# Performance work log

Hardware: AMD Instinct MI355X
Metric: run time of the kernel (lower is better)

## Reference

```python
import jax, jax.numpy as jnp
import numpy as np

B, S, D, H, FF, R, NB = 8, 1024, 768, 12, 3072, 16, 768


def _ln(x, g, b, eps=1e-6):
    m = x.mean(-1, keepdims=True)
    v = jnp.mean((x - m) ** 2, axis=-1, keepdims=True)
    return (x - m) * jax.lax.rsqrt(v + eps) * g + b


def setup_inputs() -> dict:
    key = jax.random.key(0)

    def rn(i, shape, s=0.02):
        return jax.random.normal(jax.random.fold_in(key, i), shape, jnp.float32) * s

    inp = {
        "x": jax.random.normal(jax.random.fold_in(key, 0), (B, S, D), jnp.float32),
        "attn_mask": jnp.zeros((S, S), jnp.float32),
        "norm1_g": jnp.ones((D,), jnp.float32),
        "norm1_b": jnp.zeros((D,), jnp.float32),
        "q_w": rn(1, (D, D)), "q_b": jnp.zeros((D,), jnp.float32),
        "k_w": rn(2, (D, D)), "k_b": jnp.zeros((D,), jnp.float32),
        "v_w": rn(3, (D, D)), "v_b": jnp.zeros((D,), jnp.float32),
        "o_w": rn(4, (D, D)), "o_b": jnp.zeros((D,), jnp.float32),
        "norm2_g": jnp.ones((D,), jnp.float32),
        "norm2_b": jnp.zeros((D,), jnp.float32),
        "fc1_w": rn(5, (FF, D)), "fc1_b": jnp.zeros((FF,), jnp.float32),
        "fc2_w": rn(6, (D, FF)), "fc2_b": jnp.zeros((D,), jnp.float32),
        # shared LoRA (backbone tokens)
        "lora1_A": rn(7, (D, R)), "lora1_B": rn(8, (R, FF)),
        "lora2_A": rn(9, (FF, R)), "lora2_B": rn(10, (R, D)),
        # expert VeRA: frozen shared A/B, per-expert diagonal scaling vectors
        "vera1_A": rn(11, (D, R)), "vera1_B": rn(12, (R, FF)),
        "vera2_A": rn(13, (FF, R)), "vera2_B": rn(14, (R, D)),
        "expert_fc1_d": rn(15, (R,), 1.0), "expert_fc1_b": rn(16, (FF,), 1.0),
        "expert_fc2_d": rn(17, (R,), 1.0), "expert_fc2_b": rn(18, (D,), 1.0),
        "num_backbone_tokens": NB,
    }
    return inp


def reference(x, attn_mask, norm1_g, norm1_b, q_w, q_b, k_w, k_b, v_w, v_b,
              o_w, o_b, norm2_g, norm2_b, fc1_w, fc1_b, fc2_w, fc2_b,
              lora1_A, lora1_B, lora2_A, lora2_B,
              vera1_A, vera1_B, vera2_A, vera2_B,
              expert_fc1_d, expert_fc1_b, expert_fc2_d, expert_fc2_b,
              num_backbone_tokens):
    bsz, seq, dim = x.shape
    hd = dim // H                      # head_dim = 64
    scale = hd ** -0.5
    nb = num_backbone_tokens

    # ---- attention (manual bmm + mask + softmax, eval-mode dropout = identity) ----
    h = _ln(x, norm1_g, norm1_b)
    q = (h @ q_w.T + q_b).reshape(bsz, seq, H, hd)
    k = (h @ k_w.T + k_b).reshape(bsz, seq, H, hd)
    v = (h @ v_w.T + v_b).reshape(bsz, seq, H, hd)
    scores = jnp.einsum('bqhd,bkhd->bhqk', q * scale, k) + attn_mask  # [B,H,S,S]
    probs = jax.nn.softmax(scores, axis=-1)
    ao = jnp.einsum('bhqk,bkhd->bqhd', probs, v).reshape(bsz, seq, dim)
    x = x + (ao @ o_w.T + o_b)

    # ---- MLP with split backbone (shared LoRA) / expert (VeRA) adapters ----
    residual = x
    n2 = _ln(x, norm2_g, norm2_b)
    hid = n2 @ fc1_w.T + fc1_b                                   # [B,S,FF]
    hid_b = hid[:, :nb] + (n2[:, :nb] @ lora1_A) @ lora1_B
    hid_e = hid[:, nb:] + (((n2[:, nb:] @ vera1_A) * expert_fc1_d) @ vera1_B) * expert_fc1_b
    hid = jnp.concatenate([hid_b, hid_e], axis=1)
    hid = jax.nn.gelu(hid)
    out = hid @ fc2_w.T + fc2_b                                  # [B,S,D]
    out_b = out[:, :nb] + (hid[:, :nb] @ lora2_A) @ lora2_B
    out_e = out[:, nb:] + (((hid[:, nb:] @ vera2_A) * expert_fc2_d) @ vera2_B) * expert_fc2_b
    out = jnp.concatenate([out_b, out_e], axis=1)
    return residual + out
```

## Files before the change

kernel.cpp:

```cpp
#include <hip/hip_runtime.h>
#include <stdint.h>

#define B_  8
#define S_  1024
#define D_  768
#define H_  12
#define HD_ 64
#define FF_ 3072
#define M_  (B_*S_)
#define R_  16
#define QLD 2304
#define KBLK 128

typedef unsigned short u16;
typedef short s16x8 __attribute__((ext_vector_type(8)));
typedef float fx4  __attribute__((ext_vector_type(4)));

__device__ __forceinline__ float b2f(u16 u) {
  union { unsigned int i; float f; } c; c.i = ((unsigned int)u) << 16; return c.f;
}
__device__ __forceinline__ u16 f2b(float f) {
  union { float f; unsigned int i; } c; c.f = f;
  unsigned int x = c.i;
  x += 0x7FFFu + ((x >> 16) & 1u);
  return (u16)(x >> 16);
}
__device__ __forceinline__ float gelu_f(float x) {
  float u = 0.7978845608028654f * (x + 0.044715f * x * x * x);
  float e = __expf(2.f * u);
  float t = 1.f - 2.f / (e + 1.f);
  return 0.5f * x * (1.f + t);
}
__device__ __forceinline__ void gload16(const u16* gsrc, u16* ldst) {
  __builtin_amdgcn_global_load_lds(
      (__attribute__((address_space(1))) void*)(gsrc),
      (__attribute__((address_space(3))) void*)(ldst), 16, 0, 0);
}

__global__ __launch_bounds__(256)
void cvt_all(const float* __restrict__ q_w, const float* __restrict__ k_w,
             const float* __restrict__ v_w, const float* __restrict__ o_w,
             const float* __restrict__ fc1_w, const float* __restrict__ fc2_w,
             u16* __restrict__ wqkv, u16* __restrict__ wo,
             u16* __restrict__ wfc1, u16* __restrict__ wfc2)
{
  const int i = blockIdx.x * 256 + threadIdx.x;
  const int q1  = D_ * D_ / 4;
  const int fd4 = FF_ * D_ / 4;
  const float* s; u16* d; int j;
  if      (i <     q1)       { s = q_w;   d = wqkv;            j = i; }
  else if (i < 2 * q1)       { s = k_w;   d = wqkv + D_*D_;    j = i - q1; }
  else if (i < 3 * q1)       { s = v_w;   d = wqkv + 2*D_*D_;  j = i - 2*q1; }
  else if (i < 4 * q1)       { s = o_w;   d = wo;              j = i - 3*q1; }
  else if (i < 4 * q1 + fd4) { s = fc1_w; d = wfc1;            j = i - 4*q1; }
  else                       { s = fc2_w; d = wfc2;            j = i - 4*q1 - fd4; }
  const float4 f = ((const float4*)s)[j];
  ushort4 o4; o4.x = f2b(f.x); o4.y = f2b(f.y); o4.z = f2b(f.z); o4.w = f2b(f.w);
  ((ushort4*)d)[j] = o4;
}

__global__ __launch_bounds__(256)
void prep_all(const float* __restrict__ q_bv, const float* __restrict__ k_bv,
              const float* __restrict__ v_bv, float* __restrict__ qkvb,
              const float* __restrict__ lora1B, const float* __restrict__ vera1B,
              const float* __restrict__ e1b, u16* __restrict__ up1L, u16* __restrict__ up1V,
              const float* __restrict__ lora2B, const float* __restrict__ vera2B,
              const float* __restrict__ e2b, u16* __restrict__ up2L, u16* __restrict__ up2V,
              const float* __restrict__ lora2A, const float* __restrict__ vera2A,
              u16* __restrict__ a2tL, u16* __restrict__ a2tV)
{
  const int f = blockIdx.x * 256 + threadIdx.x;
  if (f < QLD)
    qkvb[f] = (f < D_) ? q_bv[f] : (f < 2 * D_) ? k_bv[f - D_] : v_bv[f - 2 * D_];
  {
    const float ev = e1b[f];
    #pragma unroll
    for (int r = 0; r < 16; ++r) {
      up1L[(size_t)f * 32 + r] = f2b(lora1B[(size_t)r * FF_ + f]);
      up1V[(size_t)f * 32 + r] = f2b(vera1B[(size_t)r * FF_ + f] * ev);
      up1L[(size_t)f * 32 + 16 + r] = 0;
      up1V[(size_t)f * 32 + 16 + r] = 0;
    }
  }
  {
    const float4* apl = (const float4*)(lora2A + (size_t)f * 16);
    const float4* apv = (const float4*)(vera2A + (size_t)f * 16);
    #pragma unroll
    for (int q4 = 0; q4 < 4; ++q4) {
      const float4 l4 = apl[q4], v4 = apv[q4];
      a2tL[(size_t)(q4*4+0) * FF_ + f] = f2b(l4.x);
      a2tL[(size_t)(q4*4+1) * FF_ + f] = f2b(l4.y);
      a2tL[(size_t)(q4*4+2) * FF_ + f] = f2b(l4.z);
      a2tL[(size_t)(q4*4+3) * FF_ + f] = f2b(l4.w);
      a2tV[(size_t)(q4*4+0) * FF_ + f] = f2b(v4.x);
      a2tV[(size_t)(q4*4+1) * FF_ + f] = f2b(v4.y);
      a2tV[(size_t)(q4*4+2) * FF_ + f] = f2b(v4.z);
      a2tV[(size_t)(q4*4+3) * FF_ + f] = f2b(v4.w);
    }
  }
  if (f < D_) {
    const float ev = e2b[f];
    #pragma unroll
    for (int r = 0; r < 16; ++r) {
      up2L[(size_t)f * 32 + r] = f2b(lora2B[(size_t)r * D_ + f]);
      up2V[(size_t)f * 32 + r] = f2b(vera2B[(size_t)r * D_ + f] * ev);
      up2L[(size_t)f * 32 + 16 + r] = 0;
      up2V[(size_t)f * 32 + 16 + r] = 0;
    }
  }
}

template<bool ADD>
__global__ __launch_bounds__(256)
void ln_k(const float* __restrict__ x, const u16* __restrict__ add,
          const float* __restrict__ g, const float* __restrict__ beta,
          u16* __restrict__ outb, float* __restrict__ xsum,
          const float* __restrict__ Alora, const float* __restrict__ Avera,
          const float* __restrict__ dvec, u16* __restrict__ tmp1b,
          const int* __restrict__ nbp)
{
  const int row = blockIdx.x;
  const size_t base = (size_t)row * D_;
  float v0[3]; float s = 0.f, sq = 0.f;
  #pragma unroll
  for (int i = 0; i < 3; ++i) {
    const int d = threadIdx.x + i * 256;
    float val = x[base + d];
    if (ADD) { val += b2f(add[base + d]); xsum[base + d] = val; }
    v0[i] = val; s += val; sq += val * val;
  }
  #pragma unroll
  for (int mm = 32; mm >= 1; mm >>= 1) { s += __shfl_xor(s, mm); sq += __shfl_xor(sq, mm); }
  __shared__ float ss[4], s2[4];
  if ((threadIdx.x & 63) == 0) { ss[threadIdx.x >> 6] = s; s2[threadIdx.x >> 6] = sq; }
  __syncthreads();
  s  = ss[0] + ss[1] + ss[2] + ss[3];
  sq = s2[0] + s2[1] + s2[2] + s2[3];
  const float mean = s * (1.f / D_);
  const float var  = sq * (1.f / D_) - mean * mean;
  const float rs   = rsqrtf(var + 1e-6f);
  float nv[3];
  #pragma unroll
  for (int i = 0; i < 3; ++i) {
    const int d = threadIdx.x + i * 256;
    nv[i] = (v0[i] - mean) * rs * g[d] + beta[d];
    outb[base + d] = f2b(nv[i]);
  }

  if (ADD) {
    const int nb = *nbp;
    const bool ex = (row % S_) >= nb;
    const float* Am = ex ? Avera : Alora;
    float p[16];
    #pragma unroll
    for (int r = 0; r < 16; ++r) p[r] = 0.f;
    #pragma unroll
    for (int i = 0; i < 3; ++i) {
      const int d = threadIdx.x + i * 256;
      const float4* ap = (const float4*)(Am + (size_t)d * R_);
      const float4 a0 = ap[0], a1 = ap[1], a2 = ap[2], a3 = ap[3];
      const float vv = nv[i];
      p[0]  += vv * a0.x; p[1]  += vv * a0.y; p[2]  += vv * a0.z; p[3]  += vv * a0.w;
      p[4]  += vv * a1.x; p[5]  += vv * a1.y; p[6]  += vv * a1.z; p[7]  += vv * a1.w;
      p[8]  += vv * a2.x; p[9]  += vv * a2.y; p[10] += vv * a2.z; p[11] += vv * a2.w;
      p[12] += vv * a3.x; p[13] += vv * a3.y; p[14] += vv * a3.z; p[15] += vv * a3.w;
    }
    #pragma unroll
    for (int st = 1; st < 16; st <<= 1)
      #pragma unroll
      for (int r = 0; r < 16; ++r) p[r] += __shfl_xor(p[r], st);
    __shared__ float sred[16][16];
    const int grp = threadIdx.x >> 4;
    if ((threadIdx.x & 15) == 0) {
      #pragma unroll
      for (int r = 0; r < 16; ++r) sred[grp][r] = p[r];
    }
    __syncthreads();
    if (threadIdx.x < 16) {
      float v = 0.f;
      #pragma unroll
      for (int gg = 0; gg < 16; ++gg) v += sred[gg][threadIdx.x];
      if (ex) v *= dvec[threadIdx.x];
      tmp1b[(size_t)row * 32 + threadIdx.x] = f2b(v);
      tmp1b[(size_t)row * 32 + 16 + threadIdx.x] = 0;
    }
  }
}

template<int MODE>
__global__ __launch_bounds__(256)
void gemm_bt(const u16* __restrict__ A, const u16* __restrict__ W,
             const float* __restrict__ bias, u16* __restrict__ Cb,
             float* __restrict__ Cf, const float* __restrict__ resid,
             const u16* __restrict__ Aad, const u16* __restrict__ BadL,
             const u16* __restrict__ BadV, const int* __restrict__ nbp,
             int M, int N, int K)
{
  __shared__ u16 As[128 * 32];
  __shared__ u16 Bs[128 * 32];
  const int tid   = threadIdx.x;
  const int lane  = tid & 63;
  const int wid   = tid >> 6;
  const int wr    = wid >> 1;
  const int wc    = wid & 1;
  const int lr    = lane & 15;
  const int lk    = (lane >> 4) << 3;
  const int m0    = blockIdx.x * 128;
  const int n0    = blockIdx.y * 128;
  const int kg    = (tid & 3) * 8;
  const int row_a = tid >> 2;

  fx4 acc[4][4];
  const fx4 zero = {0.f, 0.f, 0.f, 0.f};
  #pragma unroll
  for (int i = 0; i < 4; ++i)
    #pragma unroll
    for (int j = 0; j < 4; ++j) acc[i][j] = zero;

  for (int k0 = 0; k0 < K; k0 += 32) {
    #pragma unroll
    for (int u = 0; u < 2; ++u) {
      const int row = u * 64 + row_a;
      const int li  = u * 256 + tid;
      gload16(A + (size_t)(m0 + row) * K + k0 + kg, &As[li * 8]);
      gload16(W + (size_t)(n0 + row) * K + k0 + kg, &Bs[li * 8]);
    }
    __syncthreads();
    s16x8 av[4], bv[4];
    #pragma unroll
    for (int i = 0; i < 4; ++i)
      av[i] = *(const s16x8*)&As[(wr * 64 + i * 16 + lr) * 32 + lk];
    #pragma unroll
    for (int j = 0; j < 4; ++j)
      bv[j] = *(const s16x8*)&Bs[(wc * 64 + j * 16 + lr) * 32 + lk];
    #pragma unroll
    for (int i = 0; i < 4; ++i)
      #pragma unroll
      for (int j = 0; j < 4; ++j)
        acc[i][j] = __builtin_amdgcn_mfma_f32_16x16x32_bf16(av[i], bv[j], acc[i][j], 0, 0, 0);
    __syncthreads();
  }

  if (MODE >= 1) {
    const int nb = *nbp;
    const u16* Bad = ((m0 % S_) >= nb) ? BadV : BadL;
    #pragma unroll
    for (int u = 0; u < 2; ++u) {
      const int row = u * 64 + row_a;
      const int li  = u * 256 + tid;
      gload16(Aad + (size_t)(m0 + row) * 32 + kg, &As[li * 8]);
      gload16(Bad + (size_t)(n0 + row) * 32 + kg, &Bs[li * 8]);
    }
    __syncthreads();
    s16x8 av[4], bv[4];
    #pragma unroll
    for (int i = 0; i < 4; ++i)
      av[i] = *(const s16x8*)&As[(wr * 64 + i * 16 + lr) * 32 + lk];
    #pragma unroll
    for (int j = 0; j < 4; ++j)
      bv[j] = *(const s16x8*)&Bs[(wc * 64 + j * 16 + lr) * 32 + lk];
    #pragma unroll
    for (int i = 0; i < 4; ++i)
      #pragma unroll
      for (int j = 0; j < 4; ++j)
        acc[i][j] = __builtin_amdgcn_mfma_f32_16x16x32_bf16(av[i], bv[j], acc[i][j], 0, 0, 0);
    __syncthreads();
  }

  const int rb = (lane >> 4) * 4;
  #pragma unroll
  for (int j = 0; j < 4; ++j) {
    const int col = n0 + wc * 64 + j * 16 + lr;
    const float bj = bias ? bias[col] : 0.f;
    #pragma unroll
    for (int i = 0; i < 4; ++i) {
      const int row = m0 + wr * 64 + i * 16 + rb;
      #pragma unroll
      for (int r = 0; r < 4; ++r) {
        const float val = acc[i][j][r] + bj;
        const size_t idx = (size_t)(row + r) * N + col;
        if (MODE == 1)      Cb[idx] = f2b(gelu_f(val));
        else if (MODE == 2) Cf[idx] = resid[idx] + val;
        else                Cb[idx] = f2b(val);
      }
    }
  }
}

__global__ __launch_bounds__(256)
void downproj(const u16* __restrict__ hid, const u16* __restrict__ A2tL,
              const u16* __restrict__ A2tV, float* __restrict__ part,
              const int* __restrict__ nbp)
{
  __shared__ u16 As[128 * 32];
  __shared__ u16 Bs[16 * 32];
  const int tid  = threadIdx.x;
  const int lane = tid & 63;
  const int w    = tid >> 6;
  const int lr   = lane & 15;
  const int lk   = (lane >> 4) << 3;
  const int m0   = blockIdx.x * 128;
  const int kb   = blockIdx.y * (FF_ / 8);
  const int nb   = *nbp;
  const u16* A2t = ((m0 % S_) >= nb) ? A2tV : A2tL;
  const int kg    = (tid & 3) * 8;
  const int row_a = tid >> 2;

  const fx4 zero = {0.f, 0.f, 0.f, 0.f};
  fx4 acc[2]; acc[0] = zero; acc[1] = zero;

  for (int k0 = kb; k0 < kb + FF_ / 8; k0 += 32) {
    #pragma unroll
    for (int u = 0; u < 2; ++u)
      gload16(hid + (size_t)(m0 + u * 64 + row_a) * FF_ + k0 + kg,
              &As[(u * 256 + tid) * 8]);
    if (tid < 64)
      gload16(A2t + (size_t)(tid >> 2) * FF_ + k0 + kg, &Bs[tid * 8]);
    __syncthreads();
    s16x8 bv = *(const s16x8*)&Bs[lr * 32 + lk];
    #pragma unroll
    for (int i = 0; i < 2; ++i) {
      s16x8 av = *(const s16x8*)&As[(w * 32 + i * 16 + lr) * 32 + lk];
      acc[i] = __builtin_amdgcn_mfma_f32_16x16x32_bf16(av, bv, acc[i], 0, 0, 0);
    }
    __syncthreads();
  }

  const int rb = (lane >> 4) * 4;
  #pragma unroll
  for (int i = 0; i < 2; ++i)
    #pragma unroll
    for (int r = 0; r < 4; ++r)
      part[(size_t)blockIdx.y * M_ * 16 +
           (size_t)(m0 + w * 32 + i * 16 + rb + r) * 16 + lr] = acc[i][r];
}

__global__ __launch_bounds__(256)
void reduce_dp(const float* __restrict__ part, const float* __restrict__ d2,
               u16* __restrict__ tmp2b, const int* __restrict__ nbp)
{
  const int idx = blockIdx.x * 256 + threadIdx.x;
  const int m = idx >> 4, r = idx & 15;
  const int nb = *nbp;
  float s = 0.f;
  #pragma unroll
  for (int ks = 0; ks < 8; ++ks) s += part[(size_t)ks * M_ * 16 + idx];
  if ((m % S_) >= nb) s *= d2[r];
  tmp2b[(size_t)m * 32 + r] = f2b(s);
  tmp2b[(size_t)m * 32 + 16 + r] = 0;
}

__global__ __launch_bounds__(256)
void attn_mfma(const u16* __restrict__ qkv, const float* __restrict__ mask,
               u16* __restrict__ o)
{
  __shared__ u16 Kl[2][128 * 64];
  __shared__ u16 Vt[2][64 * 128];
  __shared__ u16 QP[4 * 2048];

  const int tid  = threadIdx.x;
  const int lane = tid & 63;
  const int wq   = tid >> 6;
  const int lr   = lane & 15;
  const int hi   = lane >> 4;
  const int lin = blockIdx.x;
  const int vsw = (lin & 7) * 192 + (lin >> 3);
  const int qb  = vsw & 15;
  const int bh  = vsw >> 4;
  const int b    = bh / H_;
  const int h    = bh % H_;
  const size_t tok0 = (size_t)b * S_ + (size_t)qb * 64;
  const size_t colh = (size_t)h * HD_;

  const int va  = tid >> 3;
  const int vc8 = (tid & 7) * 8;

  #pragma unroll
  for (int u = 0; u < 2; ++u) {
    const int li = u * 256 + tid;
    const int r  = li >> 3;
    const int cb = ((li & 7) ^ (r & 7)) * 8;
    gload16(qkv + (tok0 + r) * QLD + colh + cb, &QP[li * 8]);
  }
  {
    const size_t ktok = (size_t)b * S_;
    #pragma unroll
    for (int u = 0; u < 4; ++u) {
      const int li = u * 256 + tid;
      const int r  = li >> 3;
      const int cb = ((li & 7) ^ (r & 7)) * 8;
      gload16(qkv + (ktok + r) * QLD + D_ + colh + cb, &Kl[0][li * 8]);
    }
    const u16* vp = qkv + (ktok + 4 * va) * QLD + 2 * D_ + colh + vc8;
    s16x8 w0 = *(const s16x8*)vp;
    s16x8 w1 = *(const s16x8*)(vp + QLD);
    s16x8 w2 = *(const s16x8*)(vp + 2 * QLD);
    s16x8 w3 = *(const s16x8*)(vp + 3 * QLD);
    #pragma unroll
    for (int jj = 0; jj < 8; ++jj) {
      const int d  = vc8 + jj;
      const int sw = ((d & 7) ^ ((d >> 3) & 7)) << 3;
      const int cp = (4 * va) ^ sw;
      *(uint32_t*)&Vt[0][d * 128 + cp] =
          (uint32_t)(u16)w0[jj] | ((uint32_t)(u16)w1[jj] << 16);
      *(uint32_t*)&Vt[0][d * 128 + cp + 2] =
          (uint32_t)(u16)w2[jj] | ((uint32_t)(u16)w3[jj] << 16);
    }
  }
  __syncthreads();

  s16x8 qa[2];
  {
    const int qrow = wq * 16 + lr;
    #pragma unroll
    for (int ks = 0; ks < 2; ++ks)
      qa[ks] = *(const s16x8*)&QP[qrow * 64 + ((ks * 32 + hi * 8) ^ ((qrow & 7) << 3))];
  }
  __syncthreads();

  const fx4 zero = {0.f, 0.f, 0.f, 0.f};
  fx4 oacc[4];
  #pragma unroll
  for (int dj = 0; dj < 4; ++dj) oacc[dj] = zero;
  float mreg[4], lreg[4];
  #pragma unroll
  for (int r = 0; r < 4; ++r) { mreg[r] = -3.0e38f; lreg[r] = 0.f; }

  const int NT = S_ / KBLK;
  for (int kt = 0; kt < NT; ++kt) {
    const int cur = kt & 1;
    const int nxt = cur ^ 1;

    s16x8 w0, w1, w2, w3;
    if (kt + 1 < NT) {
      const size_t ktokn = (size_t)b * S_ + (size_t)(kt + 1) * KBLK;
      #pragma unroll
      for (int u = 0; u < 4; ++u) {
        const int li = u * 256 + tid;
        const int r  = li >> 3;
        const int cb = ((li & 7) ^ (r & 7)) * 8;
        gload16(qkv + (ktokn + r) * QLD + D_ + colh + cb, &Kl[nxt][li * 8]);
      }
      const u16* vp = qkv + (ktokn + 4 * va) * QLD + 2 * D_ + colh + vc8;
      w0 = *(const s16x8*)vp;
      w1 = *(const s16x8*)(vp + QLD);
      w2 = *(const s16x8*)(vp + 2 * QLD);
      w3 = *(const s16x8*)(vp + 3 * QLD);
    }

    float val[8][4];
    #pragma unroll
    for (int jh = 0; jh < 2; ++jh) {
      s16x8 kb2[4][2];
      #pragma unroll
      for (int j = 0; j < 4; ++j) {
        const int n = (jh * 4 + j) * 16 + lr;
        #pragma unroll
        for (int ks = 0; ks < 2; ++ks)
          kb2[j][ks] = *(const s16x8*)&Kl[cur][n * 64 + ((ks * 32 + hi * 8) ^ ((n & 7) << 3))];
      }
      float mvh[4][4];
      {
        const float* mp = mask + (size_t)(qb * 64 + wq * 16 + hi * 4) * S_
                        + (size_t)kt * KBLK + jh * 64 + lr;
        #pragma unroll
        for (int j = 0; j < 4; ++j)
          #pragma unroll
          for (int r = 0; r < 4; ++r)
            mvh[j][r] = mp[(size_t)r * S_ + j * 16];
      }
      fx4 sf[4];
      #pragma unroll
      for (int j = 0; j < 4; ++j) sf[j] = zero;
      __builtin_amdgcn_s_setprio(1);
      #pragma unroll
      for (int ks = 0; ks < 2; ++ks)
        #pragma unroll
        for (int j = 0; j < 4; ++j)
          sf[j] = __builtin_amdgcn_mfma_f32_16x16x32_bf16(qa[ks], kb2[j][ks], sf[j], 0, 0, 0);
      __builtin_amdgcn_s_setprio(0);
      #pragma unroll
      for (int j = 0; j < 4; ++j)
        #pragma unroll
        for (int r = 0; r < 4; ++r)
          val[jh * 4 + j][r] = sf[j][r] * 0.125f + mvh[j][r];
    }

    #pragma unroll
    for (int r = 0; r < 4; ++r) {
      float mx = val[0][r];
      #pragma unroll
      for (int j = 1; j < 8; ++j) mx = fmaxf(mx, val[j][r]);
      mx = fmaxf(mx, __shfl_xor(mx, 1));
      mx = fmaxf(mx, __shfl_xor(mx, 2));
      mx = fmaxf(mx, __shfl_xor(mx, 4));
      mx = fmaxf(mx, __shfl_xor(mx, 8));
      const float mn  = fmaxf(mreg[r], mx);
      const float fac = __expf(mreg[r] - mn);
      mreg[r] = mn;
      float rs = 0.f;
      #pragma unroll
      for (int j = 0; j < 8; ++j) {
        const float p = __expf(val[j][r] - mn);
        val[j][r] = p;
        rs += p;
      }
      rs += __shfl_xor(rs, 1); rs += __shfl_xor(rs, 2);
      rs += __shfl_xor(rs, 4); rs += __shfl_xor(rs, 8);
      lreg[r] = lreg[r] * fac + rs;
      #pragma unroll
      for (int dj = 0; dj < 4; ++dj) oacc[dj][r] *= fac;
    }

    #pragma unroll
    for (int j = 0; j < 8; ++j) {
      const int col = j * 16 + lr;
      #pragma unroll
      for (int r = 0; r < 4; ++r) {
        const int row = hi * 4 + r;
        QP[wq * 2048 + row * 128 + (col ^ ((row & 7) << 3))] = f2b(val[j][r]);
      }
    }

    if (kt + 1 < NT) {
      #pragma unroll
      for (int jj = 0; jj < 8; ++jj) {
        const int d  = vc8 + jj;
        const int sw = ((d & 7) ^ ((d >> 3) & 7)) << 3;
        const int cp = (4 * va) ^ sw;
        *(uint32_t*)&Vt[nxt][d * 128 + cp] =
            (uint32_t)(u16)w0[jj] | ((uint32_t)(u16)w1[jj] << 16);
        *(uint32_t*)&Vt[nxt][d * 128 + cp + 2] =
            (uint32_t)(u16)w2[jj] | ((uint32_t)(u16)w3[jj] << 16);
      }
    }

    #pragma unroll
    for (int ks = 0; ks < 4; ++ks) {
      s16x8 pa = *(const s16x8*)&QP[wq * 2048 + lr * 128 +
                                    ((ks * 32 + hi * 8) ^ ((lr & 7) << 3))];
      s16x8 bv2[4];
      #pragma unroll
      for (int dj = 0; dj < 4; ++dj) {
        const int n  = dj * 16 + lr;
        const int sw = ((n & 7) ^ ((n >> 3) & 7)) << 3;
        bv2[dj] = *(const s16x8*)&Vt[cur][n * 128 + ((ks * 32 + hi * 8) ^ sw)];
      }
      __builtin_amdgcn_s_setprio(1);
      #pragma unroll
      for (int dj = 0; dj < 4; ++dj)
        oacc[dj] = __builtin_amdgcn_mfma_f32_16x16x32_bf16(pa, bv2[dj], oacc[dj], 0, 0, 0);
      __builtin_amdgcn_s_setprio(0);
    }

    __syncthreads();
  }

  #pragma unroll
  for (int r = 0; r < 4; ++r) {
    const float inv = 1.f / lreg[r];
    const size_t grow = (tok0 + wq * 16 + hi * 4 + r) * D_ + colh;
    #pragma unroll
    for (int dj = 0; dj < 4; ++dj)
      o[grow + dj * 16 + lr] = f2b(oacc[dj][r] * inv);
  }
}

extern "C" void kernel_launch(void* const* d_in, const int* in_sizes, int n_in,
                              void* d_out, int out_size, void* d_ws, size_t ws_size,
                              hipStream_t stream)
{
  const float* x      = (const float*)d_in[0];
  const float* mask   = (const float*)d_in[1];
  const float* n1g    = (const float*)d_in[2];
  const float* n1b    = (const float*)d_in[3];
  const float* q_w    = (const float*)d_in[4];
  const float* q_bv   = (const float*)d_in[5];
  const float* k_w    = (const float*)d_in[6];
  const float* k_bv   = (const float*)d_in[7];
  const float* v_w    = (const float*)d_in[8];
  const float* v_bv   = (const float*)d_in[9];
  const float* o_w    = (const float*)d_in[10];
  const float* o_bv   = (const float*)d_in[11];
  const float* n2g    = (const float*)d_in[12];
  const float* n2b    = (const float*)d_in[13];
  const float* fc1_w  = (const float*)d_in[14];
  const float* fc1_bv = (const float*)d_in[15];
  const float* fc2_w  = (const float*)d_in[16];
  const float* fc2_bv = (const float*)d_in[17];
  const float* lora1A = (const float*)d_in[18];
  const float* lora1B = (const float*)d_in[19];
  const float* lora2A = (const float*)d_in[20];
  const float* lora2B = (const float*)d_in[21];
  const float* vera1A = (const float*)d_in[22];
  const float* vera1B = (const float*)d_in[23];
  const float* vera2A = (const float*)d_in[24];
  const float* vera2B = (const float*)d_in[25];
  const float* e1d    = (const float*)d_in[26];
  const float* e1b    = (const float*)d_in[27];
  const float* e2d    = (const float*)d_in[28];
  const float* e2b    = (const float*)d_in[29];
  const int*   nbp    = (const int*)d_in[30];

  char* wsb = (char*)d_ws;
  u16* h1    = (u16*)wsb; wsb += (size_t)M_ * D_ * 2;
  u16* qkv   = (u16*)wsb; wsb += (size_t)M_ * QLD * 2;
  u16* attno = (u16*)wsb; wsb += (size_t)M_ * D_ * 2;
  u16* oproj = (u16*)wsb; wsb += (size_t)M_ * D_ * 2;
  u16* n2    = (u16*)wsb; wsb += (size_t)M_ * D_ * 2;
  u16* wqkv  = (u16*)wsb; wsb += (size_t)QLD * D_ * 2;
  u16* wo    = (u16*)wsb; wsb += (size_t)D_ * D_ * 2;
  u16* wfc1  = (u16*)wsb; wsb += (size_t)FF_ * D_ * 2;
  u16* wfc2  = (u16*)wsb; wsb += (size_t)D_ * FF_ * 2;
  u16* tmp1b = (u16*)wsb; wsb += (size_t)M_ * 32 * 2;
  u16* tmp2b = (u16*)wsb; wsb += (size_t)M_ * 32 * 2;
  u16* up1L  = (u16*)wsb; wsb += (size_t)FF_ * 32 * 2;
  u16* up1V  = (u16*)wsb; wsb += (size_t)FF_ * 32 * 2;
  u16* up2L  = (u16*)wsb; wsb += (size_t)D_ * 32 * 2;
  u16* up2V  = (u16*)wsb; wsb += (size_t)D_ * 32 * 2;
  u16* a2tL  = (u16*)wsb; wsb += (size_t)16 * FF_ * 2;
  u16* a2tV  = (u16*)wsb; wsb += (size_t)16 * FF_ * 2;
  float* qkvb = (float*)wsb; wsb += (size_t)QLD * 4;
  float* part = (float*)wsb; wsb += (size_t)8 * M_ * 16 * 4;
  u16* hidb = h1;

  const int totq = (4 * D_ * D_ + 2 * FF_ * D_) / 4;
  cvt_all<<<totq / 256, 256, 0, stream>>>(q_w, k_w, v_w, o_w, fc1_w, fc2_w,
                                          wqkv, wo, wfc1, wfc2);
  prep_all<<<FF_ / 256, 256, 0, stream>>>(q_bv, k_bv, v_bv, qkvb,
                                          lora1B, vera1B, e1b, up1L, up1V,
                                          lora2B, vera2B, e2b, up2L, up2V,
                                          lora2A, vera2A, a2tL, a2tV);

  ln_k<false><<<M_, 256, 0, stream>>>(x, nullptr, n1g, n1b, h1, nullptr,
                                      nullptr, nullptr, nullptr, nullptr, nullptr);
  gemm_bt<0><<<dim3(M_/128, QLD/128), 256, 0, stream>>>(
      h1, wqkv, qkvb, qkv, nullptr, nullptr, nullptr, nullptr, nullptr, nullptr,
      M_, QLD, D_);
  attn_mfma<<<(S_/64) * (B_*H_), 256, 0, stream>>>(qkv, mask, attno);
  gemm_bt<0><<<dim3(M_/128, D_/128), 256, 0, stream>>>(
      attno, wo, o_bv, oproj, nullptr, nullptr, nullptr, nullptr, nullptr, nullptr,
      M_, D_, D_);

  ln_k<true><<<M_, 256, 0, stream>>>(x, oproj, n2g, n2b, n2, (float*)d_out,
                                     lora1A, vera1A, e1d, tmp1b, nbp);

  gemm_bt<1><<<dim3(M_/128, FF_/128), 256, 0, stream>>>(
      n2, wfc1, fc1_bv, hidb, nullptr, nullptr, tmp1b, up1L, up1V, nbp,
      M_, FF_, D_);

  downproj<<<dim3(M_/128, 8), 256, 0, stream>>>(hidb, a2tL, a2tV, part, nbp);
  reduce_dp<<<M_*16/256, 256, 0, stream>>>(part, e2d, tmp2b, nbp);

  gemm_bt<2><<<dim3(M_/128, D_/128), 256, 0, stream>>>(
      hidb, wfc2, fc2_bv, nullptr, (float*)d_out, (const float*)d_out,
      tmp2b, up2L, up2V, nbp, M_, D_, FF_);
}
```

Baseline: 382.3 us.

## Transpose attention score MFMA and XCD-swizzle GEMM block mapping

The attention kernel swaps the MFMA operand order so each lane holds one query row's scores. Row max and sum then reduce mostly in registers with two cross-lane shuffles instead of four per row, and the mask loads become float4 vector reads. P is packed to bf16 with perm instructions and written as 8-byte stores into a reshaped LDS buffer. The GEMMs move to a 1D grid with a chunked swizzle that spreads consecutive blocks across the 8 XCDs for better L2 locality, at the cost of extra shuffles to broadcast rescale factors.

```diff
diff --git a/kernel.cpp b/kernel.cpp
--- a/kernel.cpp
+++ b/kernel.cpp
@@ -205,8 +205,13 @@
   const int wc    = wid & 1;
   const int lr    = lane & 15;
   const int lk    = (lane >> 4) << 3;
-  const int m0    = blockIdx.x * 128;
-  const int n0    = blockIdx.y * 128;
+  const int gn    = N >> 7;
+  const int nwg   = (M >> 7) * gn;
+  const int chunk = nwg >> 3;
+  const int lin   = blockIdx.x;
+  const int swz   = (lin & 7) * chunk + (lin >> 3);
+  const int m0    = (swz / gn) * 128;
+  const int n0    = (swz % gn) * 128;
   const int kg    = (tid & 3) * 8;
   const int row_a = tid >> 2;
 
@@ -242,8 +247,8 @@
   }
 
   if (MODE >= 1) {
-    const int nb = *nbp;
-    const u16* Bad = ((m0 % S_) >= nb) ? BadV : BadL;
+    const int nbb = *nbp;
+    const u16* Bad = ((m0 % S_) >= nbb) ? BadV : BadL;
     #pragma unroll
     for (int u = 0; u < 2; ++u) {
       const int row = u * 64 + row_a;
@@ -356,7 +361,7 @@
 {
   __shared__ u16 Kl[2][128 * 64];
   __shared__ u16 Vt[2][64 * 128];
-  __shared__ u16 QP[4 * 2048];
+  __shared__ uint32_t Pl[4][1024];
 
   const int tid  = threadIdx.x;
   const int lane = tid & 63;
@@ -374,13 +379,14 @@
 
   const int va  = tid >> 3;
   const int vc8 = (tid & 7) * 8;
+  u16* qstage = (u16*)&Pl[0][0];
 
   #pragma unroll
   for (int u = 0; u < 2; ++u) {
     const int li = u * 256 + tid;
     const int r  = li >> 3;
     const int cb = ((li & 7) ^ (r & 7)) * 8;
-    gload16(qkv + (tok0 + r) * QLD + colh + cb, &QP[li * 8]);
+    gload16(qkv + (tok0 + r) * QLD + colh + cb, &qstage[li * 8]);
   }
   {
     const size_t ktok = (size_t)b * S_;
@@ -414,7 +420,7 @@
     const int qrow = wq * 16 + lr;
     #pragma unroll
     for (int ks = 0; ks < 2; ++ks)
-      qa[ks] = *(const s16x8*)&QP[qrow * 64 + ((ks * 32 + hi * 8) ^ ((qrow & 7) << 3))];
+      qa[ks] = *(const s16x8*)&qstage[qrow * 64 + ((ks * 32 + hi * 8) ^ ((qrow & 7) << 3))];
   }
   __syncthreads();
 
@@ -422,9 +428,7 @@
   fx4 oacc[4];
   #pragma unroll
   for (int dj = 0; dj < 4; ++dj) oacc[dj] = zero;
-  float mreg[4], lreg[4];
-  #pragma unroll
-  for (int r = 0; r < 4; ++r) { mreg[r] = -3.0e38f; lreg[r] = 0.f; }
+  float mreg = -3.0e38f, lreg = 0.f;
 
   const int NT = S_ / KBLK;
   for (int kt = 0; kt < NT; ++kt) {
@@ -459,15 +463,13 @@
         for (int ks = 0; ks < 2; ++ks)
           kb2[j][ks] = *(const s16x8*)&Kl[cur][n * 64 + ((ks * 32 + hi * 8) ^ ((n & 7) << 3))];
       }
-      float mvh[4][4];
+      fx4 m4[4];
       {
-        const float* mp = mask + (size_t)(qb * 64 + wq * 16 + hi * 4) * S_
-                        + (size_t)kt * KBLK + jh * 64 + lr;
+        const float* mp = mask + (size_t)(qb * 64 + wq * 16 + lr) * S_
+                        + (size_t)kt * KBLK + jh * 64 + 4 * hi;
         #pragma unroll
         for (int j = 0; j < 4; ++j)
-          #pragma unroll
-          for (int r = 0; r < 4; ++r)
-            mvh[j][r] = mp[(size_t)r * S_ + j * 16];
+          m4[j] = *(const fx4*)(mp + j * 16);
       }
       fx4 sf[4];
       #pragma unroll
@@ -477,48 +479,58 @@
       for (int ks = 0; ks < 2; ++ks)
         #pragma unroll
         for (int j = 0; j < 4; ++j)
-          sf[j] = __builtin_amdgcn_mfma_f32_16x16x32_bf16(qa[ks], kb2[j][ks], sf[j], 0, 0, 0);
+          sf[j] = __builtin_amdgcn_mfma_f32_16x16x32_bf16(kb2[j][ks], qa[ks], sf[j], 0, 0, 0);
       __builtin_amdgcn_s_setprio(0);
       #pragma unroll
       for (int j = 0; j < 4; ++j)
         #pragma unroll
         for (int r = 0; r < 4; ++r)
-          val[jh * 4 + j][r] = sf[j][r] * 0.125f + mvh[j][r];
-    }
-
-    #pragma unroll
-    for (int r = 0; r < 4; ++r) {
-      float mx = val[0][r];
-      #pragma unroll
-      for (int j = 1; j < 8; ++j) mx = fmaxf(mx, val[j][r]);
-      mx = fmaxf(mx, __shfl_xor(mx, 1));
-      mx = fmaxf(mx, __shfl_xor(mx, 2));
-      mx = fmaxf(mx, __shfl_xor(mx, 4));
-      mx = fmaxf(mx, __shfl_xor(mx, 8));
-      const float mn  = fmaxf(mreg[r], mx);
-      const float fac = __expf(mreg[r] - mn);
-      mreg[r] = mn;
-      float rs = 0.f;
-      #pragma unroll
-      for (int j = 0; j < 8; ++j) {
-        const float p = __expf(val[j][r] - mn);
-        val[j][r] = p;
-        rs += p;
-      }
-      rs += __shfl_xor(rs, 1); rs += __shfl_xor(rs, 2);
-      rs += __shfl_xor(rs, 4); rs += __shfl_xor(rs, 8);
-      lreg[r] = lreg[r] * fac + rs;
-      #pragma unroll
-      for (int dj = 0; dj < 4; ++dj) oacc[dj][r] *= fac;
-    }
-
-    #pragma unroll
-    for (int j = 0; j < 8; ++j) {
-      const int col = j * 16 + lr;
-      #pragma unroll
-      for (int r = 0; r < 4; ++r) {
-        const int row = hi * 4 + r;
-        QP[wq * 2048 + row * 128 + (col ^ ((row & 7) << 3))] = f2b(val[j][r]);
+          val[jh * 4 + j][r] = sf[j][r] * 0.125f + m4[j][r];
+    }
+
+    {
+      float mk[8];
+      #pragma unroll
+      for (int kg = 0; kg < 8; ++kg)
+        mk[kg] = fmaxf(fmaxf(val[kg][0], val[kg][1]), fmaxf(val[kg][2], val[kg][3]));
+      float mx = fmaxf(fmaxf(fmaxf(mk[0], mk[1]), fmaxf(mk[2], mk[3])),
+                       fmaxf(fmaxf(mk[4], mk[5]), fmaxf(mk[6], mk[7])));
+      mx = fmaxf(mx, __shfl_xor(mx, 16));
+      mx = fmaxf(mx, __shfl_xor(mx, 32));
+      const float mn  = fmaxf(mreg, mx);
+      const float fac = __expf(mreg - mn);
+      mreg = mn;
+      float sk[8];
+      #pragma unroll
+      for (int kg = 0; kg < 8; ++kg) {
+        #pragma unroll
+        for (int r = 0; r < 4; ++r) val[kg][r] = __expf(val[kg][r] - mn);
+        sk[kg] = (val[kg][0] + val[kg][1]) + (val[kg][2] + val[kg][3]);
+      }
+      float rs = ((sk[0] + sk[1]) + (sk[2] + sk[3])) + ((sk[4] + sk[5]) + (sk[6] + sk[7]));
+      rs += __shfl_xor(rs, 16);
+      rs += __shfl_xor(rs, 32);
+      lreg = lreg * fac + rs;
+      float facr[4];
+      #pragma unroll
+      for (int r = 0; r < 4; ++r) facr[r] = __shfl(fac, hi * 4 + r);
+      #pragma unroll
+      for (int dj = 0; dj < 4; ++dj)
+        #pragma unroll
+        for (int r = 0; r < 4; ++r) oacc[dj][r] *= facr[r];
+    }
+
+    {
+      uint32_t* prow = &Pl[wq][lr * 64];
+      #pragma unroll
+      for (int kg = 0; kg < 8; ++kg) {
+        const uint32_t p0 = __builtin_amdgcn_perm(
+            __float_as_uint(val[kg][1]), __float_as_uint(val[kg][0]), 0x07060302u);
+        const uint32_t p1 = __builtin_amdgcn_perm(
+            __float_as_uint(val[kg][3]), __float_as_uint(val[kg][2]), 0x07060302u);
+        const int i0 = (8 * kg + 2 * hi) ^ ((lr & 7) << 3);
+        uint2 pk; pk.x = p0; pk.y = p1;
+        *(uint2*)&prow[i0] = pk;
       }
     }
 
@@ -537,8 +549,8 @@
 
     #pragma unroll
     for (int ks = 0; ks < 4; ++ks) {
-      s16x8 pa = *(const s16x8*)&QP[wq * 2048 + lr * 128 +
-                                    ((ks * 32 + hi * 8) ^ ((lr & 7) << 3))];
+      const int pbase = (16 * ks + 4 * hi) ^ ((lr & 7) << 3);
+      s16x8 pa = *(const s16x8*)&Pl[wq][lr * 64 + pbase];
       s16x8 bv2[4];
       #pragma unroll
       for (int dj = 0; dj < 4; ++dj) {
@@ -556,13 +568,18 @@
     __syncthreads();
   }
 
-  #pragma unroll
-  for (int r = 0; r < 4; ++r) {
-    const float inv = 1.f / lreg[r];
-    const size_t grow = (tok0 + wq * 16 + hi * 4 + r) * D_ + colh;
-    #pragma unroll
-    for (int dj = 0; dj < 4; ++dj)
-      o[grow + dj * 16 + lr] = f2b(oacc[dj][r] * inv);
+  {
+    const float linv = 1.f / lreg;
+    float invr[4];
+    #pragma unroll
+    for (int r = 0; r < 4; ++r) invr[r] = __shfl(linv, hi * 4 + r);
+    #pragma unroll
+    for (int r = 0; r < 4; ++r) {
+      const size_t grow = (tok0 + wq * 16 + hi * 4 + r) * D_ + colh;
+      #pragma unroll
+      for (int dj = 0; dj < 4; ++dj)
+        o[grow + dj * 16 + lr] = f2b(oacc[dj][r] * invr[r]);
+    }
   }
 }
 
@@ -634,25 +651,25 @@
 
   ln_k<false><<<M_, 256, 0, stream>>>(x, nullptr, n1g, n1b, h1, nullptr,
                                       nullptr, nullptr, nullptr, nullptr, nullptr);
-  gemm_bt<0><<<dim3(M_/128, QLD/128), 256, 0, stream>>>(
+  gemm_bt<0><<<(M_/128) * (QLD/128), 256, 0, stream>>>(
       h1, wqkv, qkvb, qkv, nullptr, nullptr, nullptr, nullptr, nullptr, nullptr,
       M_, QLD, D_);
   attn_mfma<<<(S_/64) * (B_*H_), 256, 0, stream>>>(qkv, mask, attno);
-  gemm_bt<0><<<dim3(M_/128, D_/128), 256, 0, stream>>>(
+  gemm_bt<0><<<(M_/128) * (D_/128), 256, 0, stream>>>(
       attno, wo, o_bv, oproj, nullptr, nullptr, nullptr, nullptr, nullptr, nullptr,
       M_, D_, D_);
 
   ln_k<true><<<M_, 256, 0, stream>>>(x, oproj, n2g, n2b, n2, (float*)d_out,
                                      lora1A, vera1A, e1d, tmp1b, nbp);
 
-  gemm_bt<1><<<dim3(M_/128, FF_/128), 256, 0, stream>>>(
+  gemm_bt<1><<<(M_/128) * (FF_/128), 256, 0, stream>>>(
       n2, wfc1, fc1_bv, hidb, nullptr, nullptr, tmp1b, up1L, up1V, nbp,
       M_, FF_, D_);
 
   downproj<<<dim3(M_/128, 8), 256, 0, stream>>>(hidb, a2tL, a2tV, part, nbp);
   reduce_dp<<<M_*16/256, 256, 0, stream>>>(part, e2d, tmp2b, nbp);
 
-  gemm_bt<2><<<dim3(M_/128, D_/128), 256, 0, stream>>>(
+  gemm_bt<2><<<(M_/128) * (D_/128), 256, 0, stream>>>(
       hidb, wfc2, fc2_bv, nullptr, (float*)d_out, (const float*)d_out,
       tmp2b, up2L, up2V, nbp, M_, D_, FF_);
 }
```

Measured after the change: 380.7 us. Within noise of the previous version (-0.4%).
